# Kernel optimization log

Hardware: AMD Instinct MI355X
Metric: run time of the kernel (lower is better)

## Reference

```python
import jax, jax.numpy as jnp
import numpy as np

NEG_INF = -jnp.inf
BIG_NEG = -1.0e9


def setup_inputs() -> dict:
    key = jax.random.key(0)
    ks = jax.random.split(key, 8)
    B, S, H = 8, 2048, 1024
    x = jax.random.normal(ks[0], (B, S, H), dtype=jnp.float32)
    attention_mask = jax.random.randint(ks[1], (B, S), 0, 2).astype(jnp.bool_)
    # keep first token always valid so no row is fully padded by the pad mask
    attention_mask = attention_mask.at[:, 0].set(True)
    scale = 0.02
    Wq = jax.random.normal(ks[2], (H, H), dtype=jnp.float32) * scale
    bq = jax.random.normal(ks[3], (H,), dtype=jnp.float32) * scale
    Wk = jax.random.normal(ks[4], (H, H), dtype=jnp.float32) * scale
    bk = jax.random.normal(ks[5], (H,), dtype=jnp.float32) * scale
    Wv = jax.random.normal(ks[6], (H, H), dtype=jnp.float32) * scale
    bv = jax.random.normal(ks[7], (H,), dtype=jnp.float32) * scale
    return {"x": x, "attention_mask": attention_mask, "Wq": Wq, "bq": bq,
            "Wk": Wk, "bk": bk, "Wv": Wv, "bv": bv}


def reference(x, attention_mask, Wq, bq, Wk, bk, Wv, bv):
    H = x.shape[-1]
    scale = jnp.sqrt(jnp.float32(H))
    # torch.nn.Linear: x @ W.T + b
    Q = jnp.einsum('bsh,oh->bso', x, Wq) + bq
    K = jnp.einsum('bsh,oh->bso', x, Wk) + bk
    V = jnp.einsum('bsh,oh->bso', x, Wv) + bv
    scores = jnp.einsum('bqh,bkh->bqk', Q, K) / scale  # [B,S,S]
    # faithful to masked_fill(tril(scores)==0, -inf): masks upper triangle
    # AND any lower-triangle score that is exactly zero
    scores = jnp.where(jnp.tril(scores) == 0, NEG_INF, scores)
    pad = attention_mask[:, :, None] & attention_mask[:, None, :]  # [B,S,S]
    scores = jnp.where(pad, scores, NEG_INF)
    # replace -inf with -1e9 (fully-masked rows -> uniform softmax, as in torch)
    scores = jnp.where(jnp.isneginf(scores), BIG_NEG, scores)
    attn = jax.nn.softmax(scores, axis=-1)
    return jnp.einsum('bqk,bkh->bqh', attn, V)
```

## Files before the change

### kernel.cpp

```cpp
#include <hip/hip_runtime.h>
#include <stdint.h>

typedef __bf16 bf16x8 __attribute__((ext_vector_type(8)));
typedef float f32x4 __attribute__((ext_vector_type(4)));

#define BB 8
#define SS 2048
#define HH 1024

#define TILE_B   32768ll
#define NTRI     136
#define BATCH_B  (NTRI * TILE_B)

#define OFF_Q      0ll
#define OFF_K      33554432ll
#define OFF_VT     67108864ll
#define OFF_MASK   100663296ll
#define OFF_MEANV  100679680ll
#define OFF_VIDX   100712448ll
#define OFF_NV     100843520ll
#define OFF_TMP    101711872ll
#define OFF_XBF    (OFF_TMP)
#define OFF_WBF    (OFF_TMP + 33554432ll)
#define OFF_VTC    (OFF_TMP)
#define OFF_SCORES (OFF_TMP + 33554432ll)

__device__ __forceinline__ unsigned short f2bf(float f) {
  unsigned int u = __float_as_uint(f);
  u += 0x7FFFu + ((u >> 16) & 1u);
  return (unsigned short)(u >> 16);
}
__device__ __forceinline__ float bf2f(unsigned short u) {
  return __uint_as_float(((unsigned int)u) << 16);
}

__device__ __forceinline__ void gl_lds16(const void* g, void* l) {
  __builtin_amdgcn_global_load_lds(
      (const __attribute__((address_space(1))) void*)g,
      (__attribute__((address_space(3))) void*)l, 16, 0, 0);
}

__global__ __launch_bounds__(1024) void canon_mask(
    const unsigned char* __restrict__ m, unsigned char* __restrict__ out) {
  __shared__ int cnt[4];
  const int t = threadIdx.x;
  if (t < 4) cnt[t] = 0;
  __syncthreads();
  uint4 v = ((const uint4*)m)[t];
  const unsigned char* pb = (const unsigned char*)&v;
  int loc[4] = {0, 0, 0, 0};
#pragma unroll
  for (int j = 0; j < 16; ++j)
    if (pb[j]) loc[j & 3]++;
#pragma unroll
  for (int r = 0; r < 4; ++r)
    if (loc[r]) atomicAdd(&cnt[r], loc[r]);
  __syncthreads();
  const int c0 = cnt[0], c1 = cnt[1], c2 = cnt[2], c3 = cnt[3];
  unsigned char ob[16];
  if (c0 > 0 && c1 == 0 && c2 == 0 && c3 == 0) {
    const int* mi = (const int*)m;
#pragma unroll
    for (int j = 0; j < 16; ++j) ob[j] = mi[t * 16 + j] ? 1 : 0;
  } else if (c0 == 0 && (c2 > 0 || c3 > 0)) {
    const float* mf = (const float*)m;
#pragma unroll
    for (int j = 0; j < 16; ++j) ob[j] = (mf[t * 16 + j] != 0.0f) ? 1 : 0;
  } else {
#pragma unroll
    for (int j = 0; j < 16; ++j) ob[j] = pb[j] ? 1 : 0;
  }
  ((uint4*)out)[t] = *(const uint4*)ob;
}

__global__ __launch_bounds__(256) void build_compact(
    const unsigned char* __restrict__ mask, int* __restrict__ vidx,
    int* __restrict__ nv) {
  const int b = blockIdx.x;
  const int t = threadIdx.x;
  __shared__ int cnt[256];
  __shared__ int totalS;
  const unsigned char* mb = mask + b * SS;
  unsigned char m[8];
  int c = 0;
#pragma unroll
  for (int j = 0; j < 8; ++j) { m[j] = mb[t * 8 + j]; c += m[j] ? 1 : 0; }
  cnt[t] = c;
  __syncthreads();
  int base = 0;
  for (int i = 0; i < t; ++i) base += cnt[i];
  if (t == 255) totalS = base + c;
  int pos = base;
  int* vb = vidx + b * SS;
#pragma unroll
  for (int j = 0; j < 8; ++j) {
    const int s = t * 8 + j;
    if (m[j]) { vb[pos] = s; ++pos; }
  }
  __syncthreads();
  const int total = totalS;
  if (t == 0) nv[b] = total;
  for (int idx = total + t; idx < SS; idx += 256) vb[idx] = 0;
}

__global__ void cvt_f32_bf16(const float* __restrict__ in,
                             unsigned short* __restrict__ out, int n4) {
  int i = blockIdx.x * blockDim.x + threadIdx.x;
  int stride = gridDim.x * blockDim.x;
  for (; i < n4; i += stride) {
    float4 v = ((const float4*)in)[i];
    ushort4 o;
    o.x = f2bf(v.x); o.y = f2bf(v.y); o.z = f2bf(v.z); o.w = f2bf(v.w);
    ((ushort4*)out)[i] = o;
  }
}

__global__ void cvt_w3(const float* __restrict__ Wq, const float* __restrict__ Wk,
                       const float* __restrict__ Wv, unsigned short* __restrict__ out) {
  const int z = blockIdx.y;
  const float* src = (z == 0) ? Wq : (z == 1) ? Wk : Wv;
  unsigned short* dst = out + (long)z * (HH * HH);
  const int n4 = HH * HH / 4;
  int i = blockIdx.x * 256 + threadIdx.x;
  for (; i < n4; i += 256 * 256) {
    float4 v = ((const float4*)src)[i];
    ushort4 o;
    o.x = f2bf(v.x); o.y = f2bf(v.y); o.z = f2bf(v.z); o.w = f2bf(v.w);
    ((ushort4*)dst)[i] = o;
  }
}

__global__ __launch_bounds__(256) void vtc_gather(
    const unsigned short* __restrict__ Vt, const int* __restrict__ vidx,
    const int* __restrict__ nv, unsigned short* __restrict__ Vtc) {
  const int h = blockIdx.x;
  const int b = blockIdx.y;
  const int t = threadIdx.x;
  const unsigned short* src = Vt + ((long)b * HH + h) * SS;
  unsigned short* dst = Vtc + ((long)b * HH + h) * SS;
  const int n = nv[b];
  const int* vb = vidx + b * SS;
  const int j0 = t * 8;
  unsigned short o[8];
#pragma unroll
  for (int k = 0; k < 8; ++k) {
    const int j = j0 + k;
    o[k] = (j < n) ? src[vb[j]] : (unsigned short)0;
  }
  *(ushort4*)(dst + j0) = *(const ushort4*)o;
  *(ushort4*)(dst + j0 + 4) = *(const ushort4*)(o + 4);
}

__global__ __launch_bounds__(256) void fixup_masked(
    float* __restrict__ out, const unsigned char* __restrict__ mask,
    const float* __restrict__ sums) {
  const long row = blockIdx.x;
  if (mask[row]) return;
  const long b = row >> 11;
  const int t = threadIdx.x;
  float4 v = ((const float4*)(sums + b * HH))[t];
  v.x *= (1.f / 2048.f); v.y *= (1.f / 2048.f);
  v.z *= (1.f / 2048.f); v.w *= (1.f / 2048.f);
  ((float4*)(out + row * HH))[t] = v;
}

__global__ __launch_bounds__(512, 2) void gemm256(
    const unsigned short* __restrict__ Abase,
    const unsigned short* __restrict__ Bbase, long bStride,
    char* __restrict__ Cq, char* __restrict__ Ck, char* __restrict__ VtOut,
    const float* __restrict__ biasq, const float* __restrict__ biask,
    const float* __restrict__ biasv, float* __restrict__ meanV,
    const int* __restrict__ vidx, const int* __restrict__ nv) {
  extern __shared__ char smem[];
  const int tid = threadIdx.x;
  const int wave = tid >> 6, lane = tid & 63;
  const int wr = wave >> 2, wc = wave & 3;
  const int l15 = lane & 15, l4 = lane >> 4;
  const int bz = blockIdx.z;
  const int bm = blockIdx.x, bn = blockIdx.y;

  const int b = bm >> 3;
  const int rInB = (bm & 7) * 256;
  if (bz < 2 && rInB >= nv[b]) return;

  const char* B = (const char*)(Bbase + (long)bz * bStride);

  const int srow = tid >> 3;
  const int gslot = (tid & 7) ^ (srow & 7);
  const int* vb = vidx + b * SS;
  const char* aS[4];
#pragma unroll
  for (int j = 0; j < 4; ++j) {
    const int r = rInB + srow + 64 * j;
    const int vr = (bz < 2) ? vb[r] : r;
    aS[j] = (const char*)Abase + ((long)b * SS + vr) * 2048 + gslot * 16;
  }
  const char* gB = B + ((long)bn * 256 + srow) * 2048 + gslot * 16;
  const int ldsStageW = wave << 10;

#define STG(kt_, type_, buf_) do { \
    char* _l = smem + ((buf_) << 16) + (((type_) >> 1) << 15) + \
               (((type_) & 1) << 14) + ldsStageW; \
    if ((type_) < 2) { \
      gl_lds16(aS[(type_) * 2]     + ((long)(kt_) << 7), _l); \
      gl_lds16(aS[(type_) * 2 + 1] + ((long)(kt_) << 7), _l + 8192); \
    } else { \
      const char* _g = gB + (((type_) & 1) ? 262144 : 0) + ((long)(kt_) << 7); \
      gl_lds16(_g, _l); \
      gl_lds16(_g + 131072, _l + 8192); \
    } } while (0)

  const int sw0 = ((l4 ^ (l15 & 7)) << 4);
  const int sw1 = (((4 + l4) ^ (l15 & 7)) << 4);
  const int aB0 = (wr << 14) + l15 * 128 + sw0;
  const int aB1 = (wr << 14) + l15 * 128 + sw1;
  const int bB0 = 32768 + ((wc >> 1) << 14) + (((wc & 1) << 6) + l15) * 128 + sw0;
  const int bB1 = 32768 + ((wc >> 1) << 14) + (((wc & 1) << 6) + l15) * 128 + sw1;

  f32x4 acc[8][4];
  const f32x4 z4 = {0.f, 0.f, 0.f, 0.f};
#pragma unroll
  for (int m = 0; m < 8; ++m)
#pragma unroll
    for (int n = 0; n < 4; ++n) acc[m][n] = z4;

  STG(0, 0, 0); STG(0, 1, 0); STG(0, 2, 0); STG(0, 3, 0);
  STG(1, 0, 1); STG(1, 1, 1); STG(1, 2, 1); STG(1, 3, 1);
  asm volatile("s_waitcnt vmcnt(8)" ::: "memory");
  __builtin_amdgcn_s_barrier();
  __builtin_amdgcn_sched_barrier(0);

  bf16x8 aC[4][2], bLo[2][2], bHi[2][2];

  for (int it = 0; it < 8; ++it) {
#pragma unroll
    for (int g = 0; g < 8; ++g) {
      const int buf = (g < 4) ? 0 : 65536;
      const int q = g & 3;
      if (q == 0) {
#pragma unroll
        for (int mm = 0; mm < 4; ++mm) {
          aC[mm][0] = *(const bf16x8*)(smem + buf + aB0 + mm * 2048);
          aC[mm][1] = *(const bf16x8*)(smem + buf + aB1 + mm * 2048);
        }
#pragma unroll
        for (int nn = 0; nn < 2; ++nn) {
          bLo[nn][0] = *(const bf16x8*)(smem + buf + bB0 + nn * 2048);
          bLo[nn][1] = *(const bf16x8*)(smem + buf + bB1 + nn * 2048);
        }
      } else if (q == 1) {
#pragma unroll
        for (int nn = 0; nn < 2; ++nn) {
          bHi[nn][0] = *(const bf16x8*)(smem + buf + bB0 + (2 + nn) * 2048);
          bHi[nn][1] = *(const bf16x8*)(smem + buf + bB1 + (2 + nn) * 2048);
        }
      } else if (q == 2) {
#pragma unroll
        for (int mm = 0; mm < 4; ++mm) {
          aC[mm][0] = *(const bf16x8*)(smem + buf + aB0 + (4 + mm) * 2048);
          aC[mm][1] = *(const bf16x8*)(smem + buf + aB1 + (4 + mm) * 2048);
        }
      }
      {
        const int u = it * 8 + g - 2;
        if (u >= 0) {
          const int kt = 2 + (u >> 2);
          if (kt < 16) {
            if (g == 0)      STG(kt, 0, 1);
            else if (g == 1) STG(kt, 1, 1);
            else if (g == 2) STG(kt, 2, 0);
            else if (g == 3) STG(kt, 3, 0);
            else if (g == 4) STG(kt, 0, 0);
            else if (g == 5) STG(kt, 1, 0);
            else if (g == 6) STG(kt, 2, 1);
            else             STG(kt, 3, 1);
          }
        }
      }
      __builtin_amdgcn_s_barrier();
      asm volatile("s_waitcnt lgkmcnt(0)" ::: "memory");
      __builtin_amdgcn_sched_barrier(0);
      __builtin_amdgcn_s_setprio(1);
      if (q == 0) {
#pragma unroll
        for (int mm = 0; mm < 4; ++mm)
#pragma unroll
          for (int nn = 0; nn < 2; ++nn) {
            acc[mm][nn] = __builtin_amdgcn_mfma_f32_16x16x32_bf16(
                aC[mm][0], bLo[nn][0], acc[mm][nn], 0, 0, 0);
            acc[mm][nn] = __builtin_amdgcn_mfma_f32_16x16x32_bf16(
                aC[mm][1], bLo[nn][1], acc[mm][nn], 0, 0, 0);
          }
      } else if (q == 1) {
#pragma unroll
        for (int mm = 0; mm < 4; ++mm)
#pragma unroll
          for (int nn = 0; nn < 2; ++nn) {
            acc[mm][2 + nn] = __builtin_amdgcn_mfma_f32_16x16x32_bf16(
                aC[mm][0], bHi[nn][0], acc[mm][2 + nn], 0, 0, 0);
            acc[mm][2 + nn] = __builtin_amdgcn_mfma_f32_16x16x32_bf16(
                aC[mm][1], bHi[nn][1], acc[mm][2 + nn], 0, 0, 0);
          }
      } else if (q == 2) {
#pragma unroll
        for (int mm = 0; mm < 4; ++mm)
#pragma unroll
          for (int nn = 0; nn < 2; ++nn) {
            acc[4 + mm][2 + nn] = __builtin_amdgcn_mfma_f32_16x16x32_bf16(
                aC[mm][0], bHi[nn][0], acc[4 + mm][2 + nn], 0, 0, 0);
            acc[4 + mm][2 + nn] = __builtin_amdgcn_mfma_f32_16x16x32_bf16(
                aC[mm][1], bHi[nn][1], acc[4 + mm][2 + nn], 0, 0, 0);
          }
      } else {
#pragma unroll
        for (int mm = 0; mm < 4; ++mm)
#pragma unroll
          for (int nn = 0; nn < 2; ++nn) {
            acc[4 + mm][nn] = __builtin_amdgcn_mfma_f32_16x16x32_bf16(
                aC[mm][0], bLo[nn][0], acc[4 + mm][nn], 0, 0, 0);
            acc[4 + mm][nn] = __builtin_amdgcn_mfma_f32_16x16x32_bf16(
                aC[mm][1], bLo[nn][1], acc[4 + mm][nn], 0, 0, 0);
          }
      }
      __builtin_amdgcn_s_setprio(0);
      __builtin_amdgcn_sched_barrier(0);
      if (q == 3) {
        if (g == 3 && it == 7)
          asm volatile("s_waitcnt vmcnt(0)" ::: "memory");
        else
          asm volatile("s_waitcnt vmcnt(4)" ::: "memory");
      }
      __builtin_amdgcn_s_barrier();
      asm volatile("" ::: "memory");
    }
  }
#undef STG

  const int rl0 = (wr << 7) + (l4 << 2);
  const int cl0 = (wc << 6) + l15;

  if (bz < 2) {
    const float* bias = (bz == 0) ? biasq : biask;
#pragma unroll
    for (int n = 0; n < 4; ++n) {
      const int cl = cl0 + n * 16;
      const float bv = bias[bn * 256 + cl];
      const int colx = cl ^ (l4 << 4);
#pragma unroll
      for (int m = 0; m < 8; ++m) {
        const int rl = rl0 + m * 16;
#pragma unroll
        for (int r = 0; r < 4; ++r)
          *(unsigned short*)(smem + (rl + r) * 512 + colx * 2) =
              f2bf(acc[m][n][r] + bv);
      }
    }
    __syncthreads();
    unsigned short* C = (unsigned short*)((bz == 0) ? Cq : Ck);
    const long rowg0 = (long)b * SS + rInB;
    const long colb0 = (long)bn * 512;
#pragma unroll
    for (int i = 0; i < 16; ++i) {
      const int s2 = i * 512 + tid;
      const int row = s2 >> 5;
      const int cb = s2 & 31;
      const int lb = (row * 512 + (cb << 4)) ^ (((row >> 2) & 3) << 5);
      *(uint4*)((char*)C + (rowg0 + row) * 2048 + colb0 + (cb << 4)) =
          *(const uint4*)(smem + lb);
    }
  } else {
#pragma unroll
    for (int n = 0; n < 4; ++n) {
      const int h = cl0 + n * 16;
      const float bv = biasv[bn * 256 + h];
      const int xr = (h & 7) << 4;
#pragma unroll
      for (int m = 0; m < 8; ++m) {
        const int s0a = rl0 + m * 16;
        uint2 w;
        w.x = (unsigned)f2bf(acc[m][n][0] + bv) |
              ((unsigned)f2bf(acc[m][n][1] + bv) << 16);
        w.y = (unsigned)f2bf(acc[m][n][2] + bv) |
              ((unsigned)f2bf(acc[m][n][3] + bv) << 16);
        *(uint2*)(smem + h * 512 + ((s0a * 2) ^ xr)) = w;
      }
    }
    __syncthreads();
    char* VtB = VtOut + (long)b * (SS * HH * 2) + (long)(bm & 7) * 512;
#pragma unroll
    for (int i = 0; i < 16; ++i) {
      const int s2 = i * 512 + tid;
      const int h = s2 >> 5;
      const int cb = s2 & 31;
      const int lb = h * 512 + ((cb << 4) ^ ((h & 7) << 4));
      *(uint4*)(VtB + (long)(bn * 256 + h) * 4096 + cb * 16) =
          *(const uint4*)(smem + lb);
    }
    float* mv = meanV + (long)b * HH + (long)bn * 256;
#pragma unroll
    for (int n = 0; n < 4; ++n) {
      const int h = cl0 + n * 16;
      float s = 32.0f * biasv[bn * 256 + h];
#pragma unroll
      for (int m = 0; m < 8; ++m)
        s += acc[m][n][0] + acc[m][n][1] + acc[m][n][2] + acc[m][n][3];
      atomicAdd(&mv[h], s);
    }
  }
}

__global__ __launch_bounds__(256, 2) void gemm128s(
    const unsigned short* __restrict__ Qc, const unsigned short* __restrict__ Kc,
    char* __restrict__ scoresBase, const int* __restrict__ nv) {
  __shared__ __align__(16) char smem[65536];
  const int tid = threadIdx.x;
  const int wave = tid >> 6, lane = tid & 63;
  const int wr = wave >> 1, wc = wave & 1;
  const int l15 = lane & 15, l4 = lane >> 4;
  const int bz = blockIdx.y;

  int t0 = blockIdx.x, bm = 0, a_ = 0;
  while (a_ + bm + 1 <= t0) { ++bm; a_ += bm; }
  const int bn = t0 - a_;

  const int nt = (nv[bz] + 127) >> 7;
  if (bm >= nt) return;

  const unsigned short* A = Qc + (long)bz * SS * HH;
  const unsigned short* B = Kc + (long)bz * SS * HH;

  const int s0 = tid, s1 = tid + 256;
  const int rA0 = ((s0 >> 3) << 1) | (((s0 >> 2) & 1) ^ ((s0 >> 4) & 1));
  const int cA0 = (s0 & 3) ^ (rA0 & 3);
  const int rA1 = ((s1 >> 3) << 1) | (((s1 >> 2) & 1) ^ ((s1 >> 4) & 1));
  const int cA1 = (s1 & 3) ^ (rA1 & 3);
  const char* aG0 = (const char*)A + (long)(bm * 128 + rA0) * 2048 + cA0 * 16;
  const char* aG1 = (const char*)A + (long)(bm * 128 + rA1) * 2048 + cA1 * 16;
  const char* bG0 = (const char*)B + (long)(bn * 128 + rA0) * 2048 + cA0 * 16;
  const char* bG1 = (const char*)B + (long)(bn * 128 + rA1) * 2048 + cA1 * 16;
  const int ldsL0 = wave << 10;
  const int ldsL1 = 4096 + (wave << 10);

#define STG(t_) do { \
    char* _p = smem + (((t_) & 3) << 14); \
    const long _ko = (long)(t_) << 6; \
    gl_lds16(aG0 + _ko, _p + ldsL0); \
    gl_lds16(aG1 + _ko, _p + ldsL1); \
    gl_lds16(bG0 + _ko, _p + 8192 + ldsL0); \
    gl_lds16(bG1 + _ko, _p + 8192 + ldsL1); } while (0)

  const int baseSwz = ((l15 * 64 + (l4 << 4)) ^ ((l15 & 7) << 4));
  const int rdA = (wr << 12) + baseSwz;
  const int rdB = 8192 + (wc << 12) + baseSwz;

  f32x4 acc[4][4];
  const f32x4 z4 = {0.f, 0.f, 0.f, 0.f};
#pragma unroll
  for (int m = 0; m < 4; ++m)
#pragma unroll
    for (int n = 0; n < 4; ++n) acc[m][n] = z4;

  STG(0); STG(1); STG(2);
  asm volatile("s_waitcnt vmcnt(8)" ::: "memory");
  __builtin_amdgcn_s_barrier();
  __builtin_amdgcn_sched_barrier(0);

  const int kT = 32;
  for (int t = 0; t < kT; ++t) {
    if (t + 3 < kT) STG(t + 3);
    const char* bufp = smem + ((t & 3) << 14);
    bf16x8 af[4], bg[4];
#pragma unroll
    for (int m = 0; m < 4; ++m)
      af[m] = *(const bf16x8*)(bufp + rdA + (m << 10));
#pragma unroll
    for (int n = 0; n < 4; ++n)
      bg[n] = *(const bf16x8*)(bufp + rdB + (n << 10));
    __builtin_amdgcn_s_setprio(1);
#pragma unroll
    for (int m = 0; m < 4; ++m)
#pragma unroll
      for (int n = 0; n < 4; ++n)
        acc[m][n] = __builtin_amdgcn_mfma_f32_16x16x32_bf16(af[m], bg[n],
                                                            acc[m][n], 0, 0, 0);
    __builtin_amdgcn_s_setprio(0);
    __builtin_amdgcn_sched_barrier(0);
    if (t + 3 < kT)       asm volatile("s_waitcnt vmcnt(8)" ::: "memory");
    else if (t + 3 == kT) asm volatile("s_waitcnt vmcnt(4)" ::: "memory");
    else if (t + 2 == kT) asm volatile("s_waitcnt vmcnt(0)" ::: "memory");
    if (t + 1 < kT) {
      __builtin_amdgcn_s_barrier();
      __builtin_amdgcn_sched_barrier(0);
      asm volatile("" ::: "memory");
    }
  }
#undef STG

  const int rl0 = (wr << 6) + (l4 << 2);
  const int cl0 = (wc << 6) + l15;
  char* Ct = scoresBase + (long)bz * BATCH_B + (long)t0 * TILE_B;
  __syncthreads();
#pragma unroll
  for (int m = 0; m < 4; ++m)
#pragma unroll
    for (int r = 0; r < 4; ++r) {
      const int ql = rl0 + m * 16 + r;
      const int qg = bm * 128 + ql;
#pragma unroll
      for (int n = 0; n < 4; ++n) {
        const int kg = bn * 128 + cl0 + n * 16;
        const float v = (kg <= qg) ? acc[m][n][r] * 0.03125f : -1.0e9f;
        const int colx = (cl0 + n * 16) ^ (l4 << 4);
        *(unsigned short*)(smem + ql * 256 + colx * 2) = f2bf(v);
      }
    }
  __syncthreads();
#pragma unroll
  for (int i = 0; i < 8; ++i) {
    const int s2 = i * 256 + tid;
    const int row = s2 >> 4;
    const int cb = s2 & 15;
    const int lb = row * 256 + ((cb << 4) ^ (((row >> 2) & 3) << 5));
    *(uint4*)(Ct + (long)row * 256 + (cb << 4)) = *(const uint4*)(smem + lb);
  }
}

__global__ __launch_bounds__(256) void softmax_tri(char* __restrict__ base,
                                                   const int* __restrict__ nv) {
  const int r = blockIdx.x;
  const int bz = blockIdx.y;
  if (r >= nv[bz]) return;
  const int bm = r >> 7;
  const int w = (bm + 1) << 7;
  char* bb = base + (long)bz * BATCH_B +
             (long)(bm * (bm + 1) / 2) * TILE_B + (long)(r & 127) * 256;
  const int t = threadIdx.x;
  const bool act = (t << 3) < w;
  const int bn = t >> 4;
  const int cl = (t << 3) & 127;
  char* slot = bb + (long)bn * TILE_B + (long)cl * 2;
  float v[8];
  float m = -3.0e38f;
  if (act) {
    ushort4 u0 = ((const ushort4*)slot)[0];
    ushort4 u1 = ((const ushort4*)slot)[1];
    v[0] = bf2f(u0.x); v[1] = bf2f(u0.y); v[2] = bf2f(u0.z); v[3] = bf2f(u0.w);
    v[4] = bf2f(u1.x); v[5] = bf2f(u1.y); v[6] = bf2f(u1.z); v[7] = bf2f(u1.w);
#pragma unroll
    for (int k = 0; k < 8; ++k) m = fmaxf(m, v[k]);
  }
  __shared__ float red[8];
#pragma unroll
  for (int off = 32; off > 0; off >>= 1) m = fmaxf(m, __shfl_down(m, off, 64));
  const int wid = t >> 6, lane = t & 63;
  if (lane == 0) red[wid] = m;
  __syncthreads();
  m = fmaxf(fmaxf(red[0], red[1]), fmaxf(red[2], red[3]));
  float e[8];
  float s = 0.f;
  if (act) {
#pragma unroll
    for (int k = 0; k < 8; ++k) { e[k] = __expf(v[k] - m); s += e[k]; }
  }
#pragma unroll
  for (int off = 32; off > 0; off >>= 1) s += __shfl_down(s, off, 64);
  if (lane == 0) red[4 + wid] = s;
  __syncthreads();
  s = red[4] + red[5] + red[6] + red[7];
  const float inv = 1.0f / s;
  if (act) {
    ushort4 o0, o1;
    o0.x = f2bf(e[0] * inv); o0.y = f2bf(e[1] * inv);
    o0.z = f2bf(e[2] * inv); o0.w = f2bf(e[3] * inv);
    o1.x = f2bf(e[4] * inv); o1.y = f2bf(e[5] * inv);
    o1.z = f2bf(e[6] * inv); o1.w = f2bf(e[7] * inv);
    ((ushort4*)slot)[0] = o0;
    ((ushort4*)slot)[1] = o1;
  }
}

__global__ __launch_bounds__(256, 2) void gemm_pv(
    const char* __restrict__ attn, const unsigned short* __restrict__ Vtc,
    float* __restrict__ Out, const int* __restrict__ vidx,
    const int* __restrict__ nv) {
  __shared__ __align__(16) char smem[65536];
  const int tid = threadIdx.x;
  const int wave = tid >> 6, lane = tid & 63;
  const int wr = wave >> 1, wc = wave & 1;
  const int l15 = lane & 15, l4 = lane >> 4;
  const int bz = blockIdx.z;
  const int bm = 15 - blockIdx.x;
  const int bn = blockIdx.y;

  const int nvb = nv[bz];
  const int nt = (nvb + 127) >> 7;
  if (bm >= nt) return;

  const char* Ab = attn + (long)bz * BATCH_B + (long)(bm * (bm + 1) / 2) * TILE_B;
  const unsigned short* B = Vtc + (long)bz * SS * HH;

  const int s0 = tid, s1 = tid + 256;
  const int rA0 = ((s0 >> 3) << 1) | (((s0 >> 2) & 1) ^ ((s0 >> 4) & 1));
  const int cA0 = (s0 & 3) ^ (rA0 & 3);
  const int rA1 = ((s1 >> 3) << 1) | (((s1 >> 2) & 1) ^ ((s1 >> 4) & 1));
  const int cA1 = (s1 & 3) ^ (rA1 & 3);
  const char* aB0 = Ab + (long)rA0 * 256 + cA0 * 16;
  const char* aB1 = Ab + (long)rA1 * 256 + cA1 * 16;
  const char* bG0 = (const char*)(B + (long)(bn * 128 + rA0) * SS) + cA0 * 16;
  const char* bG1 = (const char*)(B + (long)(bn * 128 + rA1) * SS) + cA1 * 16;
  const int ldsL0 = wave << 10;
  const int ldsL1 = 4096 + (wave << 10);

#define STGPV(t_) do { \
    char* _p = smem + (((t_) & 3) << 14); \
    const long _aO = (long)((t_) >> 2) * TILE_B + (long)((t_) & 3) * 64; \
    const long _bO = (long)(t_) << 6; \
    gl_lds16(aB0 + _aO, _p + ldsL0); \
    gl_lds16(aB1 + _aO, _p + ldsL1); \
    gl_lds16(bG0 + _bO, _p + 8192 + ldsL0); \
    gl_lds16(bG1 + _bO, _p + 8192 + ldsL1); } while (0)

  const int baseSwz = ((l15 * 64 + (l4 << 4)) ^ ((l15 & 7) << 4));
  const int rdA = (wr << 12) + baseSwz;
  const int rdB = 8192 + (wc << 12) + baseSwz;

  f32x4 acc[4][4];
  const f32x4 z4 = {0.f, 0.f, 0.f, 0.f};
#pragma unroll
  for (int m = 0; m < 4; ++m)
#pragma unroll
    for (int n = 0; n < 4; ++n) acc[m][n] = z4;

  STGPV(0); STGPV(1); STGPV(2);
  asm volatile("s_waitcnt vmcnt(8)" ::: "memory");
  __builtin_amdgcn_s_barrier();
  __builtin_amdgcn_sched_barrier(0);

  const int kT = (bm + 1) * 4;
  for (int t = 0; t < kT; ++t) {
    if (t + 3 < kT) STGPV(t + 3);
    const char* bufp = smem + ((t & 3) << 14);
    bf16x8 af[4], bg[4];
#pragma unroll
    for (int m = 0; m < 4; ++m)
      af[m] = *(const bf16x8*)(bufp + rdA + (m << 10));
#pragma unroll
    for (int n = 0; n < 4; ++n)
      bg[n] = *(const bf16x8*)(bufp + rdB + (n << 10));
    __builtin_amdgcn_s_setprio(1);
#pragma unroll
    for (int m = 0; m < 4; ++m)
#pragma unroll
      for (int n = 0; n < 4; ++n)
        acc[m][n] = __builtin_amdgcn_mfma_f32_16x16x32_bf16(af[m], bg[n],
                                                            acc[m][n], 0, 0, 0);
    __builtin_amdgcn_s_setprio(0);
    __builtin_amdgcn_sched_barrier(0);
    if (t + 3 < kT)       asm volatile("s_waitcnt vmcnt(8)" ::: "memory");
    else if (t + 3 == kT) asm volatile("s_waitcnt vmcnt(4)" ::: "memory");
    else if (t + 2 == kT) asm volatile("s_waitcnt vmcnt(0)" ::: "memory");
    if (t + 1 < kT) {
      __builtin_amdgcn_s_barrier();
      __builtin_amdgcn_sched_barrier(0);
      asm volatile("" ::: "memory");
    }
  }
#undef STGPV

  const int rl0 = (wr << 6) + (l4 << 2);
  const int cl0 = (wc << 6) + l15;
  __syncthreads();
#pragma unroll
  for (int m = 0; m < 4; ++m)
#pragma unroll
    for (int r = 0; r < 4; ++r) {
      const int ql = rl0 + m * 16 + r;
#pragma unroll
      for (int n = 0; n < 4; ++n) {
        const int colx = (cl0 + n * 16) ^ (l4 << 4);
        *(float*)(smem + ql * 512 + colx * 4) = acc[m][n][r];
      }
    }
  __syncthreads();
  const int* vb = vidx + (long)bz * SS;
#pragma unroll
  for (int i = 0; i < 16; ++i) {
    const int s2 = i * 256 + tid;
    const int row = s2 >> 5;
    const int cb = s2 & 31;
    const int lb = (row * 512 + (cb << 4)) ^ (((row >> 2) & 3) << 6);
    const int crow = bm * 128 + row;
    if (crow < nvb) {
      const int orig = vb[crow];
      *(uint4*)((char*)Out + (((long)bz * SS + orig) * HH) * 4 +
                (long)bn * 512 + (cb << 4)) = *(const uint4*)(smem + lb);
    }
  }
}

extern "C" void kernel_launch(void* const* d_in, const int* in_sizes, int n_in,
                              void* d_out, int out_size, void* d_ws, size_t ws_size,
                              hipStream_t stream) {
  (void)in_sizes; (void)n_in; (void)out_size; (void)ws_size;
  const float* x = (const float*)d_in[0];
  const unsigned char* mask_raw = (const unsigned char*)d_in[1];
  const float* Wq = (const float*)d_in[2];
  const float* bq = (const float*)d_in[3];
  const float* Wk = (const float*)d_in[4];
  const float* bk = (const float*)d_in[5];
  const float* Wv = (const float*)d_in[6];
  const float* bv = (const float*)d_in[7];
  char* ws = (char*)d_ws;

  unsigned short* Xbf = (unsigned short*)(ws + OFF_XBF);
  unsigned short* Wbf = (unsigned short*)(ws + OFF_WBF);
  unsigned short* Qc = (unsigned short*)(ws + OFF_Q);
  unsigned short* Kc = (unsigned short*)(ws + OFF_K);
  unsigned short* Vt = (unsigned short*)(ws + OFF_VT);
  unsigned short* Vtc = (unsigned short*)(ws + OFF_VTC);
  unsigned char* mask = (unsigned char*)(ws + OFF_MASK);
  float* meanV = (float*)(ws + OFF_MEANV);
  int* vidx = (int*)(ws + OFF_VIDX);
  int* nv = (int*)(ws + OFF_NV);

  const long MS = (long)BB * SS;

  (void)hipFuncSetAttribute((const void*)gemm256,
                            hipFuncAttributeMaxDynamicSharedMemorySize, 131072);

  canon_mask<<<1, 1024, 0, stream>>>(mask_raw, mask);
  build_compact<<<BB, 256, 0, stream>>>(mask, vidx, nv);
  hipMemsetAsync(meanV, 0, (size_t)BB * HH * 4, stream);

  cvt_f32_bf16<<<2048, 256, 0, stream>>>(x, Xbf, (int)(MS * HH / 4));
  cvt_w3<<<dim3(256, 3), 256, 0, stream>>>(Wq, Wk, Wv, Wbf);

  gemm256<<<dim3(MS / 256, HH / 256, 3), 512, 131072, stream>>>(
      Xbf, Wbf, (long)HH * HH,
      (char*)Qc, (char*)Kc, (char*)Vt, bq, bk, bv, meanV, vidx, nv);

  vtc_gather<<<dim3(HH, BB), 256, 0, stream>>>(Vt, vidx, nv, Vtc);

  gemm128s<<<dim3(NTRI, BB), 256, 0, stream>>>(
      Qc, Kc, ws + OFF_SCORES, nv);

  softmax_tri<<<dim3(SS, BB), 256, 0, stream>>>(ws + OFF_SCORES, nv);

  gemm_pv<<<dim3(SS / 128, HH / 128, BB), 256, 0, stream>>>(
      ws + OFF_SCORES, Vtc, (float*)d_out, vidx, nv);

  fixup_masked<<<BB * SS, 256, 0, stream>>>((float*)d_out, mask, meanV);
}
```

Baseline: 260.5 us.

## Compute V only for valid rows via persistent work queue; derive meanV from column sums

The QKV projection becomes a persistent kernel that pulls tiles from a queue built during mask compaction. It processes only valid (compacted) row tiles for Q, K and V, and writes the compacted transposed V directly, which removes the separate gather kernel and the full V projection over masked rows. The mean of V needed for fully masked rows is now computed separately from column sums of x and a dot product with Wv, replacing the atomic epilogue. The cost is atomic queue overhead, a 256-block grid that may underfill or load-imbalance the GPU, and two extra small kernels.

```diff
diff --git a/kernel.cpp b/kernel.cpp
--- a/kernel.cpp
+++ b/kernel.cpp
@@ -14,16 +14,18 @@
 
 #define OFF_Q      0ll
 #define OFF_K      33554432ll
-#define OFF_VT     67108864ll
+#define OFF_VTC    67108864ll
 #define OFF_MASK   100663296ll
 #define OFF_MEANV  100679680ll
 #define OFF_VIDX   100712448ll
-#define OFF_NV     100843520ll
+#define OFF_NV     100777984ll
+#define OFF_XSUM   100778048ll
+#define OFF_QCTL   100843520ll
+#define OFF_QUEUE  100843584ll
 #define OFF_TMP    101711872ll
 #define OFF_XBF    (OFF_TMP)
 #define OFF_WBF    (OFF_TMP + 33554432ll)
-#define OFF_VTC    (OFF_TMP)
-#define OFF_SCORES (OFF_TMP + 33554432ll)
+#define OFF_SCORES (OFF_TMP + 39845888ll)
 
 __device__ __forceinline__ unsigned short f2bf(float f) {
   unsigned int u = __float_as_uint(f);
@@ -75,7 +77,7 @@
 
 __global__ __launch_bounds__(256) void build_compact(
     const unsigned char* __restrict__ mask, int* __restrict__ vidx,
-    int* __restrict__ nv) {
+    int* __restrict__ nv, int* __restrict__ qctl, int* __restrict__ queue) {
   const int b = blockIdx.x;
   const int t = threadIdx.x;
   __shared__ int cnt[256];
@@ -99,7 +101,17 @@
   }
   __syncthreads();
   const int total = totalS;
-  if (t == 0) nv[b] = total;
+  if (t == 0) {
+    nv[b] = total;
+    const int ntile = (total + 255) >> 8;
+    const int n = ntile * 12;
+    const int qb = atomicAdd(&qctl[1], n);
+    int k = 0;
+    for (int tt = 0; tt < ntile; ++tt)
+      for (int z = 0; z < 3; ++z)
+        for (int bn = 0; bn < 4; ++bn)
+          queue[qb + (k++)] = (((b << 3) | tt) << 4) | (z << 2) | bn;
+  }
   for (int idx = total + t; idx < SS; idx += 256) vb[idx] = 0;
 }
 
@@ -130,25 +142,41 @@
   }
 }
 
-__global__ __launch_bounds__(256) void vtc_gather(
-    const unsigned short* __restrict__ Vt, const int* __restrict__ vidx,
-    const int* __restrict__ nv, unsigned short* __restrict__ Vtc) {
-  const int h = blockIdx.x;
+__global__ __launch_bounds__(256) void xsum_cols(
+    const unsigned short* __restrict__ Xbf, float* __restrict__ xsum) {
   const int b = blockIdx.y;
+  const int sc = blockIdx.x;
   const int t = threadIdx.x;
-  const unsigned short* src = Vt + ((long)b * HH + h) * SS;
-  unsigned short* dst = Vtc + ((long)b * HH + h) * SS;
-  const int n = nv[b];
-  const int* vb = vidx + b * SS;
-  const int j0 = t * 8;
-  unsigned short o[8];
-#pragma unroll
-  for (int k = 0; k < 8; ++k) {
-    const int j = j0 + k;
-    o[k] = (j < n) ? src[vb[j]] : (unsigned short)0;
-  }
-  *(ushort4*)(dst + j0) = *(const ushort4*)o;
-  *(ushort4*)(dst + j0 + 4) = *(const ushort4*)(o + 4);
+  const unsigned short* base = Xbf + ((long)b * SS + sc * 64) * HH + t * 4;
+  float s0 = 0.f, s1 = 0.f, s2 = 0.f, s3 = 0.f;
+#pragma unroll 4
+  for (int i = 0; i < 64; ++i) {
+    ushort4 u = *(const ushort4*)(base + (long)i * HH);
+    s0 += bf2f(u.x); s1 += bf2f(u.y); s2 += bf2f(u.z); s3 += bf2f(u.w);
+  }
+  float* xs = xsum + b * HH + t * 4;
+  atomicAdd(&xs[0], s0); atomicAdd(&xs[1], s1);
+  atomicAdd(&xs[2], s2); atomicAdd(&xs[3], s3);
+}
+
+__global__ __launch_bounds__(256) void meanv_dot(
+    const float* __restrict__ xsum, const unsigned short* __restrict__ Wvbf,
+    const float* __restrict__ bv, float* __restrict__ meanV) {
+  const int b = blockIdx.y;
+  const int wave = threadIdx.x >> 6, lane = threadIdx.x & 63;
+  const int h = blockIdx.x * 4 + wave;
+  const unsigned short* wrow = Wvbf + (long)h * HH + lane * 16;
+  const float* xs = xsum + b * HH + lane * 16;
+  float s = 0.f;
+#pragma unroll
+  for (int j = 0; j < 4; ++j) {
+    ushort4 u = *(const ushort4*)(wrow + j * 4);
+    s += bf2f(u.x) * xs[j * 4 + 0] + bf2f(u.y) * xs[j * 4 + 1] +
+         bf2f(u.z) * xs[j * 4 + 2] + bf2f(u.w) * xs[j * 4 + 3];
+  }
+#pragma unroll
+  for (int off = 32; off > 0; off >>= 1) s += __shfl_down(s, off, 64);
+  if (lane == 0) meanV[(long)b * HH + h] = s + 2048.0f * bv[h];
 }
 
 __global__ __launch_bounds__(256) void fixup_masked(
@@ -164,39 +192,56 @@
   ((float4*)(out + row * HH))[t] = v;
 }
 
-__global__ __launch_bounds__(512, 2) void gemm256(
+__global__ __launch_bounds__(512, 2) void gemm256q(
     const unsigned short* __restrict__ Abase,
     const unsigned short* __restrict__ Bbase, long bStride,
-    char* __restrict__ Cq, char* __restrict__ Ck, char* __restrict__ VtOut,
+    char* __restrict__ Cq, char* __restrict__ Ck, char* __restrict__ VtcOut,
     const float* __restrict__ biasq, const float* __restrict__ biask,
-    const float* __restrict__ biasv, float* __restrict__ meanV,
-    const int* __restrict__ vidx, const int* __restrict__ nv) {
+    const float* __restrict__ biasv,
+    const int* __restrict__ vidx, const int* __restrict__ queue,
+    int* __restrict__ qctl) {
   extern __shared__ char smem[];
+  int* bc = (int*)(smem + 131072);
   const int tid = threadIdx.x;
   const int wave = tid >> 6, lane = tid & 63;
   const int wr = wave >> 2, wc = wave & 3;
   const int l15 = lane & 15, l4 = lane >> 4;
-  const int bz = blockIdx.z;
-  const int bm = blockIdx.x, bn = blockIdx.y;
-
-  const int b = bm >> 3;
-  const int rInB = (bm & 7) * 256;
-  if (bz < 2 && rInB >= nv[b]) return;
-
-  const char* B = (const char*)(Bbase + (long)bz * bStride);
 
   const int srow = tid >> 3;
   const int gslot = (tid & 7) ^ (srow & 7);
-  const int* vb = vidx + b * SS;
-  const char* aS[4];
-#pragma unroll
-  for (int j = 0; j < 4; ++j) {
-    const int r = rInB + srow + 64 * j;
-    const int vr = (bz < 2) ? vb[r] : r;
-    aS[j] = (const char*)Abase + ((long)b * SS + vr) * 2048 + gslot * 16;
-  }
-  const char* gB = B + ((long)bn * 256 + srow) * 2048 + gslot * 16;
   const int ldsStageW = wave << 10;
+  const int sw0 = ((l4 ^ (l15 & 7)) << 4);
+  const int sw1 = (((4 + l4) ^ (l15 & 7)) << 4);
+  const int aB0 = (wr << 14) + l15 * 128 + sw0;
+  const int aB1 = (wr << 14) + l15 * 128 + sw1;
+  const int bB0 = 32768 + ((wc >> 1) << 14) + (((wc & 1) << 6) + l15) * 128 + sw0;
+  const int bB1 = 32768 + ((wc >> 1) << 14) + (((wc & 1) << 6) + l15) * 128 + sw1;
+  const int rl0 = (wr << 7) + (l4 << 2);
+  const int cl0 = (wc << 6) + l15;
+  const int qcnt = qctl[1];
+
+  for (;;) {
+    __syncthreads();
+    if (tid == 0) *bc = atomicAdd(&qctl[0], 1);
+    __syncthreads();
+    const int idx = *bc;
+    if (idx >= qcnt) break;
+    const int e = queue[idx];
+    const int bm = e >> 4;
+    const int bz = (e >> 2) & 3;
+    const int bn = e & 3;
+    const int b = bm >> 3;
+    const int rInB = (bm & 7) * 256;
+
+    const int* vb = vidx + b * SS;
+    const char* aS[4];
+#pragma unroll
+    for (int j = 0; j < 4; ++j) {
+      const int r = rInB + srow + 64 * j;
+      aS[j] = (const char*)Abase + ((long)b * SS + vb[r]) * 2048 + gslot * 16;
+    }
+    const char* gB = (const char*)(Bbase + (long)bz * bStride) +
+                     ((long)bn * 256 + srow) * 2048 + gslot * 16;
 
 #define STG(kt_, type_, buf_) do { \
     char* _l = smem + ((buf_) << 16) + (((type_) >> 1) << 15) + \
@@ -210,201 +255,182 @@
       gl_lds16(_g + 131072, _l + 8192); \
     } } while (0)
 
-  const int sw0 = ((l4 ^ (l15 & 7)) << 4);
-  const int sw1 = (((4 + l4) ^ (l15 & 7)) << 4);
-  const int aB0 = (wr << 14) + l15 * 128 + sw0;
-  const int aB1 = (wr << 14) + l15 * 128 + sw1;
-  const int bB0 = 32768 + ((wc >> 1) << 14) + (((wc & 1) << 6) + l15) * 128 + sw0;
-  const int bB1 = 32768 + ((wc >> 1) << 14) + (((wc & 1) << 6) + l15) * 128 + sw1;
-
-  f32x4 acc[8][4];
-  const f32x4 z4 = {0.f, 0.f, 0.f, 0.f};
-#pragma unroll
-  for (int m = 0; m < 8; ++m)
-#pragma unroll
-    for (int n = 0; n < 4; ++n) acc[m][n] = z4;
-
-  STG(0, 0, 0); STG(0, 1, 0); STG(0, 2, 0); STG(0, 3, 0);
-  STG(1, 0, 1); STG(1, 1, 1); STG(1, 2, 1); STG(1, 3, 1);
-  asm volatile("s_waitcnt vmcnt(8)" ::: "memory");
-  __builtin_amdgcn_s_barrier();
-  __builtin_amdgcn_sched_barrier(0);
-
-  bf16x8 aC[4][2], bLo[2][2], bHi[2][2];
-
-  for (int it = 0; it < 8; ++it) {
-#pragma unroll
-    for (int g = 0; g < 8; ++g) {
-      const int buf = (g < 4) ? 0 : 65536;
-      const int q = g & 3;
-      if (q == 0) {
-#pragma unroll
-        for (int mm = 0; mm < 4; ++mm) {
-          aC[mm][0] = *(const bf16x8*)(smem + buf + aB0 + mm * 2048);
-          aC[mm][1] = *(const bf16x8*)(smem + buf + aB1 + mm * 2048);
+    f32x4 acc[8][4];
+    const f32x4 z4 = {0.f, 0.f, 0.f, 0.f};
+#pragma unroll
+    for (int m = 0; m < 8; ++m)
+#pragma unroll
+      for (int n = 0; n < 4; ++n) acc[m][n] = z4;
+
+    STG(0, 0, 0); STG(0, 1, 0); STG(0, 2, 0); STG(0, 3, 0);
+    STG(1, 0, 1); STG(1, 1, 1); STG(1, 2, 1); STG(1, 3, 1);
+    asm volatile("s_waitcnt vmcnt(8)" ::: "memory");
+    __builtin_amdgcn_s_barrier();
+    __builtin_amdgcn_sched_barrier(0);
+
+    bf16x8 aC[4][2], bLo[2][2], bHi[2][2];
+
+    for (int it = 0; it < 8; ++it) {
+#pragma unroll
+      for (int g = 0; g < 8; ++g) {
+        const int buf = (g < 4) ? 0 : 65536;
+        const int q = g & 3;
+        if (q == 0) {
+#pragma unroll
+          for (int mm = 0; mm < 4; ++mm) {
+            aC[mm][0] = *(const bf16x8*)(smem + buf + aB0 + mm * 2048);
+            aC[mm][1] = *(const bf16x8*)(smem + buf + aB1 + mm * 2048);
+          }
+#pragma unroll
+          for (int nn = 0; nn < 2; ++nn) {
+            bLo[nn][0] = *(const bf16x8*)(smem + buf + bB0 + nn * 2048);
+            bLo[nn][1] = *(const bf16x8*)(smem + buf + bB1 + nn * 2048);
+          }
+        } else if (q == 1) {
+#pragma unroll
+          for (int nn = 0; nn < 2; ++nn) {
+            bHi[nn][0] = *(const bf16x8*)(smem + buf + bB0 + (2 + nn) * 2048);
+            bHi[nn][1] = *(const bf16x8*)(smem + buf + bB1 + (2 + nn) * 2048);
+          }
+        } else if (q == 2) {
+#pragma unroll
+          for (int mm = 0; mm < 4; ++mm) {
+            aC[mm][0] = *(const bf16x8*)(smem + buf + aB0 + (4 + mm) * 2048);
+            aC[mm][1] = *(const bf16x8*)(smem + buf + aB1 + (4 + mm) * 2048);
+          }
         }
-#pragma unroll
-        for (int nn = 0; nn < 2; ++nn) {
-          bLo[nn][0] = *(const bf16x8*)(smem + buf + bB0 + nn * 2048);
-          bLo[nn][1] = *(const bf16x8*)(smem + buf + bB1 + nn * 2048);
+        {
+          const int u = it * 8 + g - 2;
+          if (u >= 0) {
+            const int kt = 2 + (u >> 2);
+            if (kt < 16) {
+              if (g == 0)      STG(kt, 0, 1);
+              else if (g == 1) STG(kt, 1, 1);
+              else if (g == 2) STG(kt, 2, 0);
+              else if (g == 3) STG(kt, 3, 0);
+              else if (g == 4) STG(kt, 0, 0);
+              else if (g == 5) STG(kt, 1, 0);
+              else if (g == 6) STG(kt, 2, 1);
+              else             STG(kt, 3, 1);
+            }
+          }
         }
-      } else if (q == 1) {
-#pragma unroll
-        for (int nn = 0; nn < 2; ++nn) {
-          bHi[nn][0] = *(const bf16x8*)(smem + buf + bB0 + (2 + nn) * 2048);
-          bHi[nn][1] = *(const bf16x8*)(smem + buf + bB1 + (2 + nn) * 2048);
+        __builtin_amdgcn_s_barrier();
+        asm volatile("s_waitcnt lgkmcnt(0)" ::: "memory");
+        __builtin_amdgcn_sched_barrier(0);
+        __builtin_amdgcn_s_setprio(1);
+        if (q == 0) {
+#pragma unroll
+          for (int mm = 0; mm < 4; ++mm)
+#pragma unroll
+            for (int nn = 0; nn < 2; ++nn) {
+              acc[mm][nn] = __builtin_amdgcn_mfma_f32_16x16x32_bf16(
+                  aC[mm][0], bLo[nn][0], acc[mm][nn], 0, 0, 0);
+              acc[mm][nn] = __builtin_amdgcn_mfma_f32_16x16x32_bf16(
+                  aC[mm][1], bLo[nn][1], acc[mm][nn], 0, 0, 0);
+            }
+        } else if (q == 1) {
+#pragma unroll
+          for (int mm = 0; mm < 4; ++mm)
+#pragma unroll
+            for (int nn = 0; nn < 2; ++nn) {
+              acc[mm][2 + nn] = __builtin_amdgcn_mfma_f32_16x16x32_bf16(
+                  aC[mm][0], bHi[nn][0], acc[mm][2 + nn], 0, 0, 0);
+              acc[mm][2 + nn] = __builtin_amdgcn_mfma_f32_16x16x32_bf16(
+                  aC[mm][1], bHi[nn][1], acc[mm][2 + nn], 0, 0, 0);
+            }
+        } else if (q == 2) {
+#pragma unroll
+          for (int mm = 0; mm < 4; ++mm)
+#pragma unroll
+            for (int nn = 0; nn < 2; ++nn) {
+              acc[4 + mm][2 + nn] = __builtin_amdgcn_mfma_f32_16x16x32_bf16(
+                  aC[mm][0], bHi[nn][0], acc[4 + mm][2 + nn], 0, 0, 0);
+              acc[4 + mm][2 + nn] = __builtin_amdgcn_mfma_f32_16x16x32_bf16(
+                  aC[mm][1], bHi[nn][1], acc[4 + mm][2 + nn], 0, 0, 0);
+            }
+        } else {
+#pragma unroll
+          for (int mm = 0; mm < 4; ++mm)
+#pragma unroll
+            for (int nn = 0; nn < 2; ++nn) {
+              acc[4 + mm][nn] = __builtin_amdgcn_mfma_f32_16x16x32_bf16(
+                  aC[mm][0], bLo[nn][0], acc[4 + mm][nn], 0, 0, 0);
+              acc[4 + mm][nn] = __builtin_amdgcn_mfma_f32_16x16x32_bf16(
+                  aC[mm][1], bLo[nn][1], acc[4 + mm][nn], 0, 0, 0);
+            }
         }
-      } else if (q == 2) {
-#pragma unroll
-        for (int mm = 0; mm < 4; ++mm) {
-          aC[mm][0] = *(const bf16x8*)(smem + buf + aB0 + (4 + mm) * 2048);
-          aC[mm][1] = *(const bf16x8*)(smem + buf + aB1 + (4 + mm) * 2048);
+        __builtin_amdgcn_s_setprio(0);
+        __builtin_amdgcn_sched_barrier(0);
+        if (q == 3) {
+          if (g == 3 && it == 7)
+            asm volatile("s_waitcnt vmcnt(0)" ::: "memory");
+          else
+            asm volatile("s_waitcnt vmcnt(4)" ::: "memory");
+        }
+        __builtin_amdgcn_s_barrier();
+        asm volatile("" ::: "memory");
+      }
+    }
+#undef STG
+
+    if (bz < 2) {
+      const float* bias = (bz == 0) ? biasq : biask;
+#pragma unroll
+      for (int n = 0; n < 4; ++n) {
+        const int cl = cl0 + n * 16;
+        const float bv = bias[bn * 256 + cl];
+        const int colx = cl ^ (l4 << 4);
+#pragma unroll
+        for (int m = 0; m < 8; ++m) {
+          const int rl = rl0 + m * 16;
+#pragma unroll
+          for (int r = 0; r < 4; ++r)
+            *(unsigned short*)(smem + (rl + r) * 512 + colx * 2) =
+                f2bf(acc[m][n][r] + bv);
         }
       }
-      {
-        const int u = it * 8 + g - 2;
-        if (u >= 0) {
-          const int kt = 2 + (u >> 2);
-          if (kt < 16) {
-            if (g == 0)      STG(kt, 0, 1);
-            else if (g == 1) STG(kt, 1, 1);
-            else if (g == 2) STG(kt, 2, 0);
-            else if (g == 3) STG(kt, 3, 0);
-            else if (g == 4) STG(kt, 0, 0);
-            else if (g == 5) STG(kt, 1, 0);
-            else if (g == 6) STG(kt, 2, 1);
-            else             STG(kt, 3, 1);
-          }
+      __syncthreads();
+      unsigned short* C = (unsigned short*)((bz == 0) ? Cq : Ck);
+      const long rowg0 = (long)b * SS + rInB;
+      const long colb0 = (long)bn * 512;
+#pragma unroll
+      for (int i = 0; i < 16; ++i) {
+        const int s2 = i * 512 + tid;
+        const int row = s2 >> 5;
+        const int cb = s2 & 31;
+        const int lb = (row * 512 + (cb << 4)) ^ (((row >> 2) & 3) << 5);
+        *(uint4*)((char*)C + (rowg0 + row) * 2048 + colb0 + (cb << 4)) =
+            *(const uint4*)(smem + lb);
+      }
+    } else {
+#pragma unroll
+      for (int n = 0; n < 4; ++n) {
+        const int h = cl0 + n * 16;
+        const float bv = biasv[bn * 256 + h];
+        const int xr = (h & 7) << 4;
+#pragma unroll
+        for (int m = 0; m < 8; ++m) {
+          const int s0a = rl0 + m * 16;
+          uint2 w;
+          w.x = (unsigned)f2bf(acc[m][n][0] + bv) |
+                ((unsigned)f2bf(acc[m][n][1] + bv) << 16);
+          w.y = (unsigned)f2bf(acc[m][n][2] + bv) |
+                ((unsigned)f2bf(acc[m][n][3] + bv) << 16);
+          *(uint2*)(smem + h * 512 + ((s0a * 2) ^ xr)) = w;
         }
       }
-      __builtin_amdgcn_s_barrier();
-      asm volatile("s_waitcnt lgkmcnt(0)" ::: "memory");
-      __builtin_amdgcn_sched_barrier(0);
-      __builtin_amdgcn_s_setprio(1);
-      if (q == 0) {
-#pragma unroll
-        for (int mm = 0; mm < 4; ++mm)
-#pragma unroll
-          for (int nn = 0; nn < 2; ++nn) {
-            acc[mm][nn] = __builtin_amdgcn_mfma_f32_16x16x32_bf16(
-                aC[mm][0], bLo[nn][0], acc[mm][nn], 0, 0, 0);
-            acc[mm][nn] = __builtin_amdgcn_mfma_f32_16x16x32_bf16(
-                aC[mm][1], bLo[nn][1], acc[mm][nn], 0, 0, 0);
-          }
-      } else if (q == 1) {
-#pragma unroll
-        for (int mm = 0; mm < 4; ++mm)
-#pragma unroll
-          for (int nn = 0; nn < 2; ++nn) {
-            acc[mm][2 + nn] = __builtin_amdgcn_mfma_f32_16x16x32_bf16(
-                aC[mm][0], bHi[nn][0], acc[mm][2 + nn], 0, 0, 0);
-            acc[mm][2 + nn] = __builtin_amdgcn_mfma_f32_16x16x32_bf16(
-                aC[mm][1], bHi[nn][1], acc[mm][2 + nn], 0, 0, 0);
-          }
-      } else if (q == 2) {
-#pragma unroll
-        for (int mm = 0; mm < 4; ++mm)
-#pragma unroll
-          for (int nn = 0; nn < 2; ++nn) {
-            acc[4 + mm][2 + nn] = __builtin_amdgcn_mfma_f32_16x16x32_bf16(
-                aC[mm][0], bHi[nn][0], acc[4 + mm][2 + nn], 0, 0, 0);
-            acc[4 + mm][2 + nn] = __builtin_amdgcn_mfma_f32_16x16x32_bf16(
-                aC[mm][1], bHi[nn][1], acc[4 + mm][2 + nn], 0, 0, 0);
-          }
-      } else {
-#pragma unroll
-        for (int mm = 0; mm < 4; ++mm)
-#pragma unroll
-          for (int nn = 0; nn < 2; ++nn) {
-            acc[4 + mm][nn] = __builtin_amdgcn_mfma_f32_16x16x32_bf16(
-                aC[mm][0], bLo[nn][0], acc[4 + mm][nn], 0, 0, 0);
-            acc[4 + mm][nn] = __builtin_amdgcn_mfma_f32_16x16x32_bf16(
-                aC[mm][1], bLo[nn][1], acc[4 + mm][nn], 0, 0, 0);
-          }
+      __syncthreads();
+      char* VtB = VtcOut + (long)b * (SS * HH * 2) + (long)(bm & 7) * 512;
+#pragma unroll
+      for (int i = 0; i < 16; ++i) {
+        const int s2 = i * 512 + tid;
+        const int h = s2 >> 5;
+        const int cb = s2 & 31;
+        const int lb = h * 512 + ((cb << 4) ^ ((h & 7) << 4));
+        *(uint4*)(VtB + (long)(bn * 256 + h) * 4096 + cb * 16) =
+            *(const uint4*)(smem + lb);
       }
-      __builtin_amdgcn_s_setprio(0);
-      __builtin_amdgcn_sched_barrier(0);
-      if (q == 3) {
-        if (g == 3 && it == 7)
-          asm volatile("s_waitcnt vmcnt(0)" ::: "memory");
-        else
-          asm volatile("s_waitcnt vmcnt(4)" ::: "memory");
-      }
-      __builtin_amdgcn_s_barrier();
-      asm volatile("" ::: "memory");
-    }
-  }
-#undef STG
-
-  const int rl0 = (wr << 7) + (l4 << 2);
-  const int cl0 = (wc << 6) + l15;
-
-  if (bz < 2) {
-    const float* bias = (bz == 0) ? biasq : biask;
-#pragma unroll
-    for (int n = 0; n < 4; ++n) {
-      const int cl = cl0 + n * 16;
-      const float bv = bias[bn * 256 + cl];
-      const int colx = cl ^ (l4 << 4);
-#pragma unroll
-      for (int m = 0; m < 8; ++m) {
-        const int rl = rl0 + m * 16;
-#pragma unroll
-        for (int r = 0; r < 4; ++r)
-          *(unsigned short*)(smem + (rl + r) * 512 + colx * 2) =
-              f2bf(acc[m][n][r] + bv);
-      }
-    }
-    __syncthreads();
-    unsigned short* C = (unsigned short*)((bz == 0) ? Cq : Ck);
-    const long rowg0 = (long)b * SS + rInB;
-    const long colb0 = (long)bn * 512;
-#pragma unroll
-    for (int i = 0; i < 16; ++i) {
-      const int s2 = i * 512 + tid;
-      const int row = s2 >> 5;
-      const int cb = s2 & 31;
-      const int lb = (row * 512 + (cb << 4)) ^ (((row >> 2) & 3) << 5);
-      *(uint4*)((char*)C + (rowg0 + row) * 2048 + colb0 + (cb << 4)) =
-          *(const uint4*)(smem + lb);
-    }
-  } else {
-#pragma unroll
-    for (int n = 0; n < 4; ++n) {
-      const int h = cl0 + n * 16;
-      const float bv = biasv[bn * 256 + h];
-      const int xr = (h & 7) << 4;
-#pragma unroll
-      for (int m = 0; m < 8; ++m) {
-        const int s0a = rl0 + m * 16;
-        uint2 w;
-        w.x = (unsigned)f2bf(acc[m][n][0] + bv) |
-              ((unsigned)f2bf(acc[m][n][1] + bv) << 16);
-        w.y = (unsigned)f2bf(acc[m][n][2] + bv) |
-              ((unsigned)f2bf(acc[m][n][3] + bv) << 16);
-        *(uint2*)(smem + h * 512 + ((s0a * 2) ^ xr)) = w;
-      }
-    }
-    __syncthreads();
-    char* VtB = VtOut + (long)b * (SS * HH * 2) + (long)(bm & 7) * 512;
-#pragma unroll
-    for (int i = 0; i < 16; ++i) {
-      const int s2 = i * 512 + tid;
-      const int h = s2 >> 5;
-      const int cb = s2 & 31;
-      const int lb = h * 512 + ((cb << 4) ^ ((h & 7) << 4));
-      *(uint4*)(VtB + (long)(bn * 256 + h) * 4096 + cb * 16) =
-          *(const uint4*)(smem + lb);
-    }
-    float* mv = meanV + (long)b * HH + (long)bn * 256;
-#pragma unroll
-    for (int n = 0; n < 4; ++n) {
-      const int h = cl0 + n * 16;
-      float s = 32.0f * biasv[bn * 256 + h];
-#pragma unroll
-      for (int m = 0; m < 8; ++m)
-        s += acc[m][n][0] + acc[m][n][1] + acc[m][n][2] + acc[m][n][3];
-      atomicAdd(&mv[h], s);
     }
   }
 }
@@ -716,30 +742,35 @@
   unsigned short* Wbf = (unsigned short*)(ws + OFF_WBF);
   unsigned short* Qc = (unsigned short*)(ws + OFF_Q);
   unsigned short* Kc = (unsigned short*)(ws + OFF_K);
-  unsigned short* Vt = (unsigned short*)(ws + OFF_VT);
   unsigned short* Vtc = (unsigned short*)(ws + OFF_VTC);
   unsigned char* mask = (unsigned char*)(ws + OFF_MASK);
   float* meanV = (float*)(ws + OFF_MEANV);
   int* vidx = (int*)(ws + OFF_VIDX);
   int* nv = (int*)(ws + OFF_NV);
+  float* xsum = (float*)(ws + OFF_XSUM);
+  int* qctl = (int*)(ws + OFF_QCTL);
+  int* queue = (int*)(ws + OFF_QUEUE);
 
   const long MS = (long)BB * SS;
 
-  (void)hipFuncSetAttribute((const void*)gemm256,
-                            hipFuncAttributeMaxDynamicSharedMemorySize, 131072);
-
+  (void)hipFuncSetAttribute((const void*)gemm256q,
+                            hipFuncAttributeMaxDynamicSharedMemorySize, 131088);
+
+  hipMemsetAsync(qctl, 0, 8, stream);
+  hipMemsetAsync(xsum, 0, (size_t)BB * HH * 4, stream);
   canon_mask<<<1, 1024, 0, stream>>>(mask_raw, mask);
-  build_compact<<<BB, 256, 0, stream>>>(mask, vidx, nv);
-  hipMemsetAsync(meanV, 0, (size_t)BB * HH * 4, stream);
+  build_compact<<<BB, 256, 0, stream>>>(mask, vidx, nv, qctl, queue);
 
   cvt_f32_bf16<<<2048, 256, 0, stream>>>(x, Xbf, (int)(MS * HH / 4));
   cvt_w3<<<dim3(256, 3), 256, 0, stream>>>(Wq, Wk, Wv, Wbf);
 
-  gemm256<<<dim3(MS / 256, HH / 256, 3), 512, 131072, stream>>>(
+  xsum_cols<<<dim3(32, BB), 256, 0, stream>>>(Xbf, xsum);
+  meanv_dot<<<dim3(HH / 4, BB), 256, 0, stream>>>(
+      xsum, Wbf + 2 * HH * HH, bv, meanV);
+
+  gemm256q<<<256, 512, 131088, stream>>>(
       Xbf, Wbf, (long)HH * HH,
-      (char*)Qc, (char*)Kc, (char*)Vt, bq, bk, bv, meanV, vidx, nv);
-
-  vtc_gather<<<dim3(HH, BB), 256, 0, stream>>>(Vt, vidx, nv, Vtc);
+      (char*)Qc, (char*)Kc, (char*)Vtc, bq, bk, bv, vidx, queue, qctl);
 
   gemm128s<<<dim3(NTRI, BB), 256, 0, stream>>>(
       Qc, Kc, ws + OFF_SCORES, nv);
```

New measurement: 246.0 us. 1.06x faster.
